# Optimization experiments

Measured on AMD Instinct MI355X. Metric: run time of the kernel, lower is better.

## Reference

```python
import jax, jax.numpy as jnp
import numpy as np

B, A, N, D = 512, 3, 64, 32


def _lte(x):
    """LTETransform: straight-through hard threshold (forward: 1[x>0], backward: identity)."""
    hard = (x > 0).astype(x.dtype)
    return x + jax.lax.stop_gradient(hard - x)


def setup_inputs() -> dict:
    key = jax.random.key(0)
    k1, k2 = jax.random.split(key)
    feature = jax.random.normal(k1, (B, N, D), dtype=jnp.float32)
    indicator = jax.random.normal(k2, (A, N, D), dtype=jnp.float32)
    return {"feature": feature, "indicator": indicator}


def reference(feature, indicator):
    # gate = LTE(DotWeight(indicator[0], indicator[1])) -> [N, N]
    gate = _lte(jnp.einsum('id,jd->ij', indicator[0], indicator[1]))

    # QKV[a,i,j,:,:] = indicator[a,i,:] (outer) indicator[a,j,:]  (rank-1), so
    # input[b,a,i,j,d] = (feature[b,i,:] . indicator[a,i,:]) * indicator[a,j,d]
    s = jnp.einsum('bnd,and->ban', feature, indicator)  # [B, 3, N]

    # query[b,i,j,d] = elu(s[b,0,i] * ind[0,j,d]) + 1              [B,N,N,D]
    q = jax.nn.elu(s[:, 0, :, None, None] * indicator[0][None, None, :, :]) + 1.0
    # key.transpose(1,2)[b,i,j,d] = elu(s[b,1,j] * ind[1,i,d]) + 1  [B,N,N,D]
    k_t = jax.nn.elu(s[:, 1, None, :, None] * indicator[1][None, :, None, :]) + 1.0

    score = jnp.einsum('bijd,bijd->bij', q, k_t)  # [B, N, N]
    probs = jax.nn.softmax(score, axis=-1)
    score_hat = probs * gate[None, :, :]

    # value[b,i,j,d] = s[b,2,i] * ind[2,j,d];  out = sum_j scoreHat * value
    out = s[:, 2, :, None] * jnp.einsum('bij,jd->bid', score_hat, indicator[2])
    return out  # [B, N, D]
```

## Files before the change

### kernel.cpp

```cpp
#include <hip/hip_runtime.h>

namespace {
constexpr int N  = 64;
constexpr int D  = 32;
constexpr int PD = 36;
constexpr int SHP = 68;
constexpr float LOG2E = 1.4426950408889634f;
constexpr float LN2   = 0.6931471805599453f;

#if __has_builtin(__builtin_amdgcn_exp2f)
__device__ __forceinline__ float fexp2(float x) { return __builtin_amdgcn_exp2f(x); }
#else
__device__ __forceinline__ float fexp2(float x) { return exp2f(x); }
#endif
#if __has_builtin(__builtin_amdgcn_rcpf)
__device__ __forceinline__ float frcp(float x) { return __builtin_amdgcn_rcpf(x); }
#else
__device__ __forceinline__ float frcp(float x) { return 1.0f / x; }
#endif

__device__ __forceinline__ float elup1_scaled(float xL) {
    return fmaf(fmaxf(xL, 0.f), LN2, fexp2(fminf(xL, 0.f)));
}

__global__ __launch_bounds__(512, 6) void fused(
        const float* __restrict__ feature,
        const float* __restrict__ ind,
        float* __restrict__ out) {
    __shared__ float ind_lds[3][N][PD];
    __shared__ float s_lds[3][N];
    __shared__ float gate_lds[32][N];
    __shared__ float sh_lds[32][SHP];

    const int t    = threadIdx.x;
    const int lane = t & 63;
    const int wave = t >> 6;
    const int blk  = blockIdx.x;
    const int b    = blk >> 1;
    const int i_base = (blk & 1) * 32;

    {
        const float4* src = reinterpret_cast<const float4*>(ind);
#pragma unroll
        for (int idx = t; idx < 3 * N * D / 4; idx += 512) {
            int a = idx >> 9;
            int r = idx & 511;
            int n = r >> 3;
            int k = r & 7;
            *reinterpret_cast<float4*>(&ind_lds[a][n][k * 4]) = src[idx];
        }
    }
    __syncthreads();

    {
        const int i_loc = t >> 4;
        const int jq    = t & 15;
        float4 acc = {0.f, 0.f, 0.f, 0.f};
#pragma unroll
        for (int dq = 0; dq < 8; ++dq) {
            float4 a4 = *reinterpret_cast<const float4*>(&ind_lds[0][i_base + i_loc][dq * 4]);
#pragma unroll
            for (int c = 0; c < 4; ++c) {
                float4 b4 = *reinterpret_cast<const float4*>(&ind_lds[1][jq + 16 * c][dq * 4]);
                (&acc.x)[c] += a4.x * b4.x + a4.y * b4.y + a4.z * b4.z + a4.w * b4.w;
            }
        }
#pragma unroll
        for (int c = 0; c < 4; ++c)
            gate_lds[i_loc][jq + 16 * c] = ((&acc.x)[c] > 0.f) ? 1.f : 0.f;

        if (t < 3 * N) {
            int a = t >> 6, n = t & 63;
            const float4* frow = reinterpret_cast<const float4*>(feature + ((size_t)b * N + n) * D);
            float sa = 0.f;
#pragma unroll
            for (int k = 0; k < 8; ++k) {
                float4 f4 = frow[k];
                float4 i4 = *reinterpret_cast<const float4*>(&ind_lds[a][n][k * 4]);
                sa += f4.x * i4.x + f4.y * i4.y + f4.z * i4.z + f4.w * i4.w;
            }
            s_lds[a][n] = sa;
        }
    }
    __syncthreads();

    float4 u[8];
#pragma unroll
    for (int k = 0; k < 8; ++k)
        u[k] = *reinterpret_cast<const float4*>(&ind_lds[0][lane][k * 4]);
    const float s1jL = s_lds[1][lane] * LOG2E;

#pragma unroll 1
    for (int r = 0; r < 4; ++r) {
        const int   i_loc = wave * 4 + r;
        const int   ig    = i_base + i_loc;
        const float s0iL  = s_lds[0][ig] * LOG2E;
        const float s2i   = s_lds[2][ig];

        float score = 0.f;
#pragma unroll
        for (int k = 0; k < 8; ++k) {
            float4 v4 = *reinterpret_cast<const float4*>(&ind_lds[1][ig][k * 4]);
#pragma unroll
            for (int c = 0; c < 4; ++c) {
                float q  = elup1_scaled(s0iL * (&u[k].x)[c]);
                float kt = elup1_scaled(s1jL * (&v4.x)[c]);
                score = fmaf(q, kt, score);
            }
        }

        float m = score;
#pragma unroll
        for (int off = 32; off >= 1; off >>= 1) m = fmaxf(m, __shfl_xor(m, off));
        float e = fexp2((score - m) * LOG2E);
        float ssum = e;
#pragma unroll
        for (int off = 32; off >= 1; off >>= 1) ssum += __shfl_xor(ssum, off);

        float g   = gate_lds[i_loc][lane];
        float shv = (e * g) * (frcp(ssum) * s2i);
        sh_lds[i_loc][lane] = shv;
    }
    __syncthreads();

    {
        const int i_loc = t >> 4;
        const int sub   = t & 15;
        const int dq    = sub & 7;
        const int jh    = sub >> 3;
        float4 acc = {0.f, 0.f, 0.f, 0.f};
#pragma unroll
        for (int jj = 0; jj < 32; jj += 4) {
            int j = jh * 32 + jj;
            float4 sh4 = *reinterpret_cast<const float4*>(&sh_lds[i_loc][j]);
#pragma unroll
            for (int c = 0; c < 4; ++c) {
                float4 v4 = *reinterpret_cast<const float4*>(&ind_lds[2][j + c][dq * 4]);
                float  w  = (&sh4.x)[c];
                acc.x = fmaf(w, v4.x, acc.x);
                acc.y = fmaf(w, v4.y, acc.y);
                acc.z = fmaf(w, v4.z, acc.z);
                acc.w = fmaf(w, v4.w, acc.w);
            }
        }
        acc.x += __shfl_xor(acc.x, 8);
        acc.y += __shfl_xor(acc.y, 8);
        acc.z += __shfl_xor(acc.z, 8);
        acc.w += __shfl_xor(acc.w, 8);
        if (jh == 0) {
            *reinterpret_cast<float4*>(out + ((size_t)b * N + i_base + i_loc) * D + dq * 4) = acc;
        }
    }
}
}

extern "C" void kernel_launch(void* const* d_in, const int* in_sizes, int n_in,
                              void* d_out, int out_size, void* d_ws, size_t ws_size,
                              hipStream_t stream) {
    const float* feature = (const float*)d_in[0];
    const float* ind     = (const float*)d_in[1];
    float*       out     = (float*)d_out;
    fused<<<1024, 512, 0, stream>>>(feature, ind, out);
}
```

Measured before the change: 88.81 us.

## Process whole batch per block, batch four softmax rows, merge ELU exponentials

Each block now handles all 64 rows of one batch instead of half, which halves the grid and removes the redundant per-block indicator load and gate compute. The score loop merges the two ELU exponentials into a single exp2 of the summed negative parts, reducing transcendental count. Softmax reductions are interleaved across four rows for more ILP. The exp2/rcp intrinsics are replaced by library calls and a true division, and the occupancy hint drops to 4. The added per-block work and lower block count may reduce latency hiding.

```diff
diff --git a/kernel.cpp b/kernel.cpp
--- a/kernel.cpp
+++ b/kernel.cpp
@@ -3,41 +3,27 @@
 namespace {
 constexpr int N  = 64;
 constexpr int D  = 32;
-constexpr int PD = 36;
+constexpr int PD  = 36;
 constexpr int SHP = 68;
 constexpr float LOG2E = 1.4426950408889634f;
 constexpr float LN2   = 0.6931471805599453f;
 
-#if __has_builtin(__builtin_amdgcn_exp2f)
-__device__ __forceinline__ float fexp2(float x) { return __builtin_amdgcn_exp2f(x); }
-#else
 __device__ __forceinline__ float fexp2(float x) { return exp2f(x); }
-#endif
-#if __has_builtin(__builtin_amdgcn_rcpf)
-__device__ __forceinline__ float frcp(float x) { return __builtin_amdgcn_rcpf(x); }
-#else
-__device__ __forceinline__ float frcp(float x) { return 1.0f / x; }
-#endif
+__device__ __forceinline__ float frcp(float x) { return __frcp_rn(x) * 1.0f; }
 
-__device__ __forceinline__ float elup1_scaled(float xL) {
-    return fmaf(fmaxf(xL, 0.f), LN2, fexp2(fminf(xL, 0.f)));
-}
-
-__global__ __launch_bounds__(512, 6) void fused(
+__global__ __launch_bounds__(512, 4) void fused(
         const float* __restrict__ feature,
         const float* __restrict__ ind,
         float* __restrict__ out) {
     __shared__ float ind_lds[3][N][PD];
     __shared__ float s_lds[3][N];
-    __shared__ float gate_lds[32][N];
-    __shared__ float sh_lds[32][SHP];
+    __shared__ float gate_lds[N][N];
+    __shared__ float sh_lds[N][SHP];
 
     const int t    = threadIdx.x;
     const int lane = t & 63;
     const int wave = t >> 6;
-    const int blk  = blockIdx.x;
-    const int b    = blk >> 1;
-    const int i_base = (blk & 1) * 32;
+    const int b    = blockIdx.x;
 
     {
         const float4* src = reinterpret_cast<const float4*>(ind);
@@ -53,21 +39,21 @@
     __syncthreads();
 
     {
-        const int i_loc = t >> 4;
-        const int jq    = t & 15;
-        float4 acc = {0.f, 0.f, 0.f, 0.f};
+        const int i  = t >> 3;
+        const int jq = t & 7;
+        float acc[8] = {0.f, 0.f, 0.f, 0.f, 0.f, 0.f, 0.f, 0.f};
 #pragma unroll
         for (int dq = 0; dq < 8; ++dq) {
-            float4 a4 = *reinterpret_cast<const float4*>(&ind_lds[0][i_base + i_loc][dq * 4]);
+            float4 a4 = *reinterpret_cast<const float4*>(&ind_lds[0][i][dq * 4]);
 #pragma unroll
-            for (int c = 0; c < 4; ++c) {
-                float4 b4 = *reinterpret_cast<const float4*>(&ind_lds[1][jq + 16 * c][dq * 4]);
-                (&acc.x)[c] += a4.x * b4.x + a4.y * b4.y + a4.z * b4.z + a4.w * b4.w;
+            for (int c = 0; c < 8; ++c) {
+                float4 b4 = *reinterpret_cast<const float4*>(&ind_lds[1][jq + 8 * c][dq * 4]);
+                acc[c] += a4.x * b4.x + a4.y * b4.y + a4.z * b4.z + a4.w * b4.w;
             }
         }
 #pragma unroll
-        for (int c = 0; c < 4; ++c)
-            gate_lds[i_loc][jq + 16 * c] = ((&acc.x)[c] > 0.f) ? 1.f : 0.f;
+        for (int c = 0; c < 8; ++c)
+            gate_lds[i][jq + 8 * c] = (acc[c] > 0.f) ? 1.f : 0.f;
 
         if (t < 3 * N) {
             int a = t >> 6, n = t & 63;
@@ -88,51 +74,65 @@
 #pragma unroll
     for (int k = 0; k < 8; ++k)
         u[k] = *reinterpret_cast<const float4*>(&ind_lds[0][lane][k * 4]);
-    const float s1jL = s_lds[1][lane] * LOG2E;
+    const float s1L = s_lds[1][lane] * LOG2E;
 
 #pragma unroll 1
-    for (int r = 0; r < 4; ++r) {
-        const int   i_loc = wave * 4 + r;
-        const int   ig    = i_base + i_loc;
-        const float s0iL  = s_lds[0][ig] * LOG2E;
-        const float s2i   = s_lds[2][ig];
-
-        float score = 0.f;
+    for (int g = 0; g < 2; ++g) {
+        const int i0 = wave * 8 + g * 4;
+        float score[4];
 #pragma unroll
-        for (int k = 0; k < 8; ++k) {
-            float4 v4 = *reinterpret_cast<const float4*>(&ind_lds[1][ig][k * 4]);
+        for (int r = 0; r < 4; ++r) {
+            const int   ig  = i0 + r;
+            const float s0L = s_lds[0][ig] * LOG2E;
+            float sc = 0.f;
 #pragma unroll
-            for (int c = 0; c < 4; ++c) {
-                float q  = elup1_scaled(s0iL * (&u[k].x)[c]);
-                float kt = elup1_scaled(s1jL * (&v4.x)[c]);
-                score = fmaf(q, kt, score);
+            for (int k = 0; k < 8; ++k) {
+                float4 v4 = *reinterpret_cast<const float4*>(&ind_lds[1][ig][k * 4]);
+#pragma unroll
+                for (int c = 0; c < 4; ++c) {
+                    float aL = s0L * (&u[k].x)[c];
+                    float bL = s1L * (&v4.x)[c];
+                    float E  = fexp2(fminf(aL, 0.f) + fminf(bL, 0.f));
+                    float A  = fmaf(fmaxf(aL, 0.f), LN2, 1.0f);
+                    float B  = fmaf(fmaxf(bL, 0.f), LN2, 1.0f);
+                    sc = fmaf(E * A, B, sc);
+                }
             }
+            score[r] = sc;
         }
 
-        float m = score;
+        float mx[4], e[4], sm[4];
 #pragma unroll
-        for (int off = 32; off >= 1; off >>= 1) m = fmaxf(m, __shfl_xor(m, off));
-        float e = fexp2((score - m) * LOG2E);
-        float ssum = e;
+        for (int r = 0; r < 4; ++r) mx[r] = score[r];
 #pragma unroll
-        for (int off = 32; off >= 1; off >>= 1) ssum += __shfl_xor(ssum, off);
-
-        float g   = gate_lds[i_loc][lane];
-        float shv = (e * g) * (frcp(ssum) * s2i);
-        sh_lds[i_loc][lane] = shv;
+        for (int off = 32; off >= 1; off >>= 1) {
+#pragma unroll
+            for (int r = 0; r < 4; ++r) mx[r] = fmaxf(mx[r], __shfl_xor(mx[r], off));
+        }
+#pragma unroll
+        for (int r = 0; r < 4; ++r) e[r] = fexp2((score[r] - mx[r]) * LOG2E);
+#pragma unroll
+        for (int r = 0; r < 4; ++r) sm[r] = e[r];
+#pragma unroll
+        for (int off = 32; off >= 1; off >>= 1) {
+#pragma unroll
+            for (int r = 0; r < 4; ++r) sm[r] += __shfl_xor(sm[r], off);
+        }
+#pragma unroll
+        for (int r = 0; r < 4; ++r) {
+            const int ig = i0 + r;
+            sh_lds[ig][lane] = (e[r] * gate_lds[ig][lane]) * (s_lds[2][ig] / sm[r]);
+        }
     }
     __syncthreads();
 
     {
-        const int i_loc = t >> 4;
-        const int sub   = t & 15;
-        const int dq    = sub & 7;
-        const int jh    = sub >> 3;
+        const int i  = t >> 3;
+        const int dq = t & 7;
         float4 acc = {0.f, 0.f, 0.f, 0.f};
-#pragma unroll
-        for (int jj = 0; jj < 32; jj += 4) {
-            int j = jh * 32 + jj;
-            float4 sh4 = *reinterpret_cast<const float4*>(&sh_lds[i_loc][j]);
+#pragma unroll 4
+        for (int j = 0; j < N; j += 4) {
+            float4 sh4 = *reinterpret_cast<const float4*>(&sh_lds[i][j]);
 #pragma unroll
             for (int c = 0; c < 4; ++c) {
                 float4 v4 = *reinterpret_cast<const float4*>(&ind_lds[2][j + c][dq * 4]);
@@ -143,13 +143,7 @@
                 acc.w = fmaf(w, v4.w, acc.w);
             }
         }
-        acc.x += __shfl_xor(acc.x, 8);
-        acc.y += __shfl_xor(acc.y, 8);
-        acc.z += __shfl_xor(acc.z, 8);
-        acc.w += __shfl_xor(acc.w, 8);
-        if (jh == 0) {
-            *reinterpret_cast<float4*>(out + ((size_t)b * N + i_base + i_loc) * D + dq * 4) = acc;
-        }
+        *reinterpret_cast<float4*>(out + ((size_t)b * N + i) * D + dq * 4) = acc;
     }
 }
 }
@@ -160,5 +154,5 @@
     const float* feature = (const float*)d_in[0];
     const float* ind     = (const float*)d_in[1];
     float*       out     = (float*)d_out;
-    fused<<<1024, 512, 0, stream>>>(feature, ind, out);
+    fused<<<512, 512, 0, stream>>>(feature, ind, out);
 }
```

New measurement: 98.04 us. +10.4%, slower.
